# Kernel tuning notes

Hardware: AMD Instinct MI355X
Metric: run time of the kernel (lower is better)

Reference implementation:

```python
import jax, jax.numpy as jnp
import numpy as np

B, S, H, D = 4, 2048, 16, 128  # batch, seq_len, heads, head_dim
ADJ_SCALE = 0.1


def setup_inputs() -> dict:
    key = jax.random.key(0)
    k1, k2, k3 = jax.random.split(key, 3)
    x = jax.random.normal(k1, (B, S, H, D), dtype=jnp.float32)
    W = jax.random.normal(k2, (D, D), dtype=jnp.float32) * (1.0 / np.sqrt(D))
    b = jax.random.normal(k3, (D,), dtype=jnp.float32) * 0.02
    return {"x": x, "W": W, "b": b}


def reference(x, W, b):
    Bq, Sq, Hq, Dq = x.shape
    # ---- betweenness over [B*H, S, D] ----
    xc = jnp.transpose(x, (0, 2, 1, 3)).reshape(Bq * Hq, Sq, Dq)
    content = jnp.einsum('nsd,ed->nse', xc, W) + b  # Linear(dim, dim)
    # only the (i,i+1) and (i,i+2) distance bands are consumed by the loop
    d01 = jnp.linalg.norm(content[:, :-1] - content[:, 1:], axis=-1)   # [N, S-1]
    d02 = jnp.linalg.norm(content[:, :-2] - content[:, 2:], axis=-1)   # [N, S-2]
    direct = d02
    path = d01[:, :-1] + d01[:, 1:]
    score = jax.nn.relu(1.0 - (path - direct) / jnp.maximum(direct, 1e-6))  # [N, S-2]
    between = jnp.zeros((Bq * Hq, Sq), x.dtype).at[:, 1:Sq - 1].set(score / (Sq - 2))
    between = jnp.transpose(between.reshape(Bq, Hq, Sq), (0, 2, 1))  # [B, S, H]
    # ---- RoPE freq tables ----
    base = 1.0 / (10000.0 ** (jnp.arange(0, Dq, 2, dtype=jnp.float32) / Dq))
    freqs = jnp.arange(Sq, dtype=jnp.float32)[:, None] * base[None, :]  # [S, D/2]
    fcos, fsin = jnp.cos(freqs), jnp.sin(freqs)
    # ---- betweenness-adjusted interpolated RoPE ----
    pos_adj = (between - 0.5) * ADJ_SCALE                               # [B, S, H]
    adj_pos = jnp.clip(jnp.arange(Sq, dtype=jnp.float32)[None, :, None] + pos_adj,
                       0.0, Sq - 1)
    lo = jnp.floor(adj_pos).astype(jnp.int32)
    hi = jnp.ceil(adj_pos).astype(jnp.int32)
    frac = (adj_pos - lo)[..., None]                                    # [B, S, H, 1]
    cos_i = (1.0 - frac) * fcos[lo] + frac * fcos[hi]                   # [B, S, H, D/2]
    sin_i = (1.0 - frac) * fsin[lo] + frac * fsin[hi]
    xe, xo = x[..., 0::2], x[..., 1::2]
    oe = xe * cos_i - xo * sin_i
    oo = xo * cos_i + xe * sin_i
    return jnp.stack([oe, oo], axis=-1).reshape(x.shape)
```

## Files before the change

kernel.cpp:

```cpp
#include <hip/hip_runtime.h>
#include <hip/hip_bf16.h>
#include <math.h>

#define S_LEN 2048
#define NH    64
#define TS    62
#define NTILE 33

typedef __attribute__((ext_vector_type(8))) short short8;
typedef __attribute__((ext_vector_type(4))) float f32x4;

__device__ __forceinline__ unsigned short f2bf(float f) {
    unsigned int u = __float_as_uint(f);
    return (unsigned short)((u + 0x7FFFu + ((u >> 16) & 1u)) >> 16);
}

__global__ __launch_bounds__(256) void k_misc(const float* __restrict__ W,
                                              unsigned short* __restrict__ Wbf,
                                              float* __restrict__ fcos,
                                              float* __restrict__ fsin)
{
    int bid = blockIdx.x;
    if (bid < 512) {
        int tid = bid * 256 + threadIdx.x;
        int j = tid & 63;
        int s = tid >> 6;
        float base = powf(10000.f, -(float)(2 * j) * (1.f / 128.f));
        float fr = (float)s * base;
        fcos[tid] = cosf(fr);
        fsin[tid] = sinf(fr);
    } else {
        int idx = (bid - 512) * 256 + threadIdx.x;
        Wbf[idx] = f2bf(W[idx]);
    }
}

__global__ __launch_bounds__(256) void k_dist(const float* __restrict__ x,
                                              const unsigned short* __restrict__ Wbf,
                                              float* __restrict__ d01,
                                              float* __restrict__ d02)
{
    __shared__ char smem[52224];
    unsigned short* Xs  = (unsigned short*)smem;
    unsigned short* Wsh = (unsigned short*)(smem + 17408);
    float*          Cs  = (float*)smem;

    const int tile = blockIdx.x;
    const int n    = blockIdx.y;
    const int bb   = n >> 4, hh = n & 15;
    const int s0   = tile * TS;
    const int t    = threadIdx.x;
    const int w    = t >> 6;
    const int l    = t & 63;
    const int m    = l & 15;
    const int q    = l >> 4;

    #pragma unroll
    for (int i = 0; i < 8; i++) {
        int idx = t + 256 * i;
        int r   = idx >> 5;
        int c4  = idx & 31;
        float4 v = *(const float4*)&x[(((size_t)(bb * S_LEN + s0 + r) * 16 + hh)) * 128 + c4 * 4];
        ushort4 p;
        p.x = f2bf(v.x); p.y = f2bf(v.y); p.z = f2bf(v.z); p.w = f2bf(v.w);
        *(ushort4*)&Xs[r * 136 + c4 * 4] = p;
    }
    #pragma unroll
    for (int i = 0; i < 8; i++) {
        int idx = t + 256 * i;
        int r   = idx >> 4;
        int c8  = idx & 15;
        uint4 v = *(const uint4*)&Wbf[r * 128 + c8 * 8];
        *(uint4*)&Wsh[r * 136 + c8 * 8] = v;
    }
    __syncthreads();

    f32x4 acc[8];
    #pragma unroll
    for (int ct = 0; ct < 8; ct++) acc[ct] = (f32x4){0.f, 0.f, 0.f, 0.f};

    #pragma unroll
    for (int kk = 0; kk < 4; kk++) {
        short8 a = *(const short8*)&Xs[(16 * w + m) * 136 + kk * 32 + q * 8];
        #pragma unroll
        for (int ct = 0; ct < 8; ct++) {
            short8 b = *(const short8*)&Wsh[(16 * ct + m) * 136 + kk * 32 + q * 8];
            acc[ct] = __builtin_amdgcn_mfma_f32_16x16x32_bf16(a, b, acc[ct], 0, 0, 0);
        }
    }
    __syncthreads();

    #pragma unroll
    for (int ct = 0; ct < 8; ct++) {
        int col   = 16 * ct + m;
        int rbase = 16 * w + q * 4;
        #pragma unroll
        for (int r = 0; r < 4; r++)
            Cs[col * 65 + rbase + r] = acc[ct][r];
    }
    __syncthreads();

    int which = w >> 1;
    int j     = (w & 1) * 32 + (l >> 1);
    int g     = l & 1;
    int lim   = which ? (TS - 1) : TS;
    bool active = (j <= lim);
    float part = 0.f;
    if (active) {
        int r1 = j, r2 = j + 1 + which;
        #pragma unroll 8
        for (int i = 0; i < 64; i++) {
            int e = g + 2 * i;
            float d = Cs[e * 65 + r1] - Cs[e * 65 + r2];
            part += d * d;
        }
    }
    part += __shfl_xor(part, 1);
    if (active && g == 0) {
        float dv = sqrtf(part);
        if (which == 0) d01[n * S_LEN + s0 + j] = dv;
        else            d02[n * S_LEN + s0 + j] = dv;
    }
}

__global__ __launch_bounds__(256) void k_between(const float* __restrict__ d01,
                                                 const float* __restrict__ d02,
                                                 float* __restrict__ bet)
{
    int tid = blockIdx.x * 256 + threadIdx.x;
    if (tid >= 4 * S_LEN * 16) return;
    int h = tid & 15;
    int s = (tid >> 4) & (S_LEN - 1);
    int b = tid >> 15;
    float v = 0.f;
    if (s >= 1 && s <= S_LEN - 2) {
        int nn = b * 16 + h;
        int i = s - 1;
        float p  = d01[nn * S_LEN + i] + d01[nn * S_LEN + i + 1];
        float dd = d02[nn * S_LEN + i];
        float sc = 1.f - (p - dd) / fmaxf(dd, 1e-6f);
        v = fmaxf(sc, 0.f) * (1.f / (float)(S_LEN - 2));
    }
    bet[tid] = v;
}

__global__ __launch_bounds__(256) void k_rope(const float* __restrict__ x,
                                              const float* __restrict__ bet,
                                              const float* __restrict__ fcos,
                                              const float* __restrict__ fsin,
                                              float* __restrict__ out)
{
    int tid = blockIdx.x * 256 + threadIdx.x;
    int j = tid & 63;
    int s = (tid >> 10) & (S_LEN - 1);

    float between = bet[tid >> 6];
    float adj = (float)s + (between - 0.5f) * 0.1f;
    adj = fminf(fmaxf(adj, 0.f), (float)(S_LEN - 1));
    float lo = floorf(adj), hi = ceilf(adj);
    float frac = adj - lo;
    int li = (int)lo, hii = (int)hi;

    float cl = fcos[li * 64 + j],  ch = fcos[hii * 64 + j];
    float sl = fsin[li * 64 + j],  sh = fsin[hii * 64 + j];
    float ci = (1.f - frac) * cl + frac * ch;
    float si = (1.f - frac) * sl + frac * sh;

    float2 xv = ((const float2*)x)[tid];
    float oe = xv.x * ci - xv.y * si;
    float oo = xv.y * ci + xv.x * si;
    ((float2*)out)[tid] = make_float2(oe, oo);
}

extern "C" void kernel_launch(void* const* d_in, const int* in_sizes, int n_in,
                              void* d_out, int out_size, void* d_ws, size_t ws_size,
                              hipStream_t stream)
{
    const float* x = (const float*)d_in[0];
    const float* W = (const float*)d_in[1];
    float* out = (float*)d_out;

    float* ws   = (float*)d_ws;
    float* d01  = ws;
    float* d02  = ws + 131072;
    float* bet  = ws + 262144;
    float* fcos = ws + 393216;
    float* fsin = ws + 524288;
    unsigned short* Wbf = (unsigned short*)(ws + 655360);

    k_misc   <<<576, 256, 0, stream>>>(W, Wbf, fcos, fsin);
    k_dist   <<<dim3(NTILE, NH), 256, 0, stream>>>(x, Wbf, d01, d02);
    k_between<<<512,  256, 0, stream>>>(d01, d02, bet);
    k_rope   <<<32768, 256, 0, stream>>>(x, bet, fcos, fsin, out);
}
```

Before: 145.1 us.

## Fuse betweenness into RoPE kernel, interleave cos/sin table, vectorize to float4

The separate betweenness kernel is removed and its score is recomputed inline inside the RoPE kernel, which drops one launch and the intermediate buffer. The cos and sin tables are interleaved into one float2 table so a single float4 load fetches both values for two frequencies. Each thread now handles four output floats with float4 loads and stores, halving the grid. In exchange, every thread redundantly reads d01/d02 for its (b,s,h) row, though these reads should mostly be cache hits.

```diff
diff --git a/kernel.cpp b/kernel.cpp
--- a/kernel.cpp
+++ b/kernel.cpp
@@ -17,8 +17,7 @@
 
 __global__ __launch_bounds__(256) void k_misc(const float* __restrict__ W,
                                               unsigned short* __restrict__ Wbf,
-                                              float* __restrict__ fcos,
-                                              float* __restrict__ fsin)
+                                              float2* __restrict__ tab)
 {
     int bid = blockIdx.x;
     if (bid < 512) {
@@ -27,8 +26,7 @@
         int s = tid >> 6;
         float base = powf(10000.f, -(float)(2 * j) * (1.f / 128.f));
         float fr = (float)s * base;
-        fcos[tid] = cosf(fr);
-        fsin[tid] = sinf(fr);
+        tab[tid] = make_float2(cosf(fr), sinf(fr));
     } else {
         int idx = (bid - 512) * 256 + threadIdx.x;
         Wbf[idx] = f2bf(W[idx]);
@@ -123,53 +121,49 @@
     }
 }
 
-__global__ __launch_bounds__(256) void k_between(const float* __restrict__ d01,
-                                                 const float* __restrict__ d02,
-                                                 float* __restrict__ bet)
+__global__ __launch_bounds__(256) void k_rope4(const float* __restrict__ x,
+                                               const float* __restrict__ d01,
+                                               const float* __restrict__ d02,
+                                               const float2* __restrict__ tab,
+                                               float* __restrict__ out)
 {
-    int tid = blockIdx.x * 256 + threadIdx.x;
-    if (tid >= 4 * S_LEN * 16) return;
-    int h = tid & 15;
-    int s = (tid >> 4) & (S_LEN - 1);
-    int b = tid >> 15;
-    float v = 0.f;
+    int tid4 = blockIdx.x * 256 + threadIdx.x;
+    int d4   = tid4 & 31;
+    int rem  = tid4 >> 5;
+    int h    = rem & 15;
+    int s    = (rem >> 4) & (S_LEN - 1);
+    int b    = rem >> 15;
+    int n    = b * 16 + h;
+
+    float bet = 0.f;
     if (s >= 1 && s <= S_LEN - 2) {
-        int nn = b * 16 + h;
         int i = s - 1;
-        float p  = d01[nn * S_LEN + i] + d01[nn * S_LEN + i + 1];
-        float dd = d02[nn * S_LEN + i];
+        float p  = d01[n * S_LEN + i] + d01[n * S_LEN + i + 1];
+        float dd = d02[n * S_LEN + i];
         float sc = 1.f - (p - dd) / fmaxf(dd, 1e-6f);
-        v = fmaxf(sc, 0.f) * (1.f / (float)(S_LEN - 2));
+        bet = fmaxf(sc, 0.f) * (1.f / (float)(S_LEN - 2));
     }
-    bet[tid] = v;
-}
 
-__global__ __launch_bounds__(256) void k_rope(const float* __restrict__ x,
-                                              const float* __restrict__ bet,
-                                              const float* __restrict__ fcos,
-                                              const float* __restrict__ fsin,
-                                              float* __restrict__ out)
-{
-    int tid = blockIdx.x * 256 + threadIdx.x;
-    int j = tid & 63;
-    int s = (tid >> 10) & (S_LEN - 1);
+    float adj = (float)s + (bet - 0.5f) * 0.1f;
+    adj = fminf(fmaxf(adj, 0.f), (float)(S_LEN - 1));
+    float lof = floorf(adj), hif = ceilf(adj);
+    float frac = adj - lof;
+    int lo = (int)lof, hi = (int)hif;
 
-    float between = bet[tid >> 6];
-    float adj = (float)s + (between - 0.5f) * 0.1f;
-    adj = fminf(fmaxf(adj, 0.f), (float)(S_LEN - 1));
-    float lo = floorf(adj), hi = ceilf(adj);
-    float frac = adj - lo;
-    int li = (int)lo, hii = (int)hi;
+    float4 tl = *(const float4*)&tab[lo * 64 + 2 * d4];
+    float4 th = *(const float4*)&tab[hi * 64 + 2 * d4];
+    float ci0 = (1.f - frac) * tl.x + frac * th.x;
+    float si0 = (1.f - frac) * tl.y + frac * th.y;
+    float ci1 = (1.f - frac) * tl.z + frac * th.z;
+    float si1 = (1.f - frac) * tl.w + frac * th.w;
 
-    float cl = fcos[li * 64 + j],  ch = fcos[hii * 64 + j];
-    float sl = fsin[li * 64 + j],  sh = fsin[hii * 64 + j];
-    float ci = (1.f - frac) * cl + frac * ch;
-    float si = (1.f - frac) * sl + frac * sh;
-
-    float2 xv = ((const float2*)x)[tid];
-    float oe = xv.x * ci - xv.y * si;
-    float oo = xv.y * ci + xv.x * si;
-    ((float2*)out)[tid] = make_float2(oe, oo);
+    float4 xv = ((const float4*)x)[tid4];
+    float4 o;
+    o.x = xv.x * ci0 - xv.y * si0;
+    o.y = xv.y * ci0 + xv.x * si0;
+    o.z = xv.z * ci1 - xv.w * si1;
+    o.w = xv.w * ci1 + xv.z * si1;
+    ((float4*)out)[tid4] = o;
 }
 
 extern "C" void kernel_launch(void* const* d_in, const int* in_sizes, int n_in,
@@ -180,16 +174,13 @@
     const float* W = (const float*)d_in[1];
     float* out = (float*)d_out;
 
-    float* ws   = (float*)d_ws;
-    float* d01  = ws;
-    float* d02  = ws + 131072;
-    float* bet  = ws + 262144;
-    float* fcos = ws + 393216;
-    float* fsin = ws + 524288;
-    unsigned short* Wbf = (unsigned short*)(ws + 655360);
+    float* ws = (float*)d_ws;
+    float* d01 = ws;
+    float* d02 = ws + 131072;
+    float2* tab = (float2*)(ws + 262144);
+    unsigned short* Wbf = (unsigned short*)(ws + 524288);
 
-    k_misc   <<<576, 256, 0, stream>>>(W, Wbf, fcos, fsin);
-    k_dist   <<<dim3(NTILE, NH), 256, 0, stream>>>(x, Wbf, d01, d02);
-    k_between<<<512,  256, 0, stream>>>(d01, d02, bet);
-    k_rope   <<<32768, 256, 0, stream>>>(x, bet, fcos, fsin, out);
+    k_misc <<<576, 256, 0, stream>>>(W, Wbf, tab);
+    k_dist <<<dim3(NTILE, NH), 256, 0, stream>>>(x, Wbf, d01, d02);
+    k_rope4<<<16384, 256, 0, stream>>>(x, d01, d02, tab, out);
 }
```

Result: faster. 137.1 us (-5.6%).
